# Performance work log

Measured on AMD Instinct MI355X. Metric: run time of the kernel, lower is better.

Reference implementation:

```python
import jax, jax.numpy as jnp
import numpy as np

EMB = 1024; H = 8; HD = EMB // H // 2  # head_dim = 64, q/k use 2*H heads of HD; v uses H heads of 2*HD
FF = 4096; DEPTH = 1
LAM_INIT = float(0.8 - 0.6 * np.exp(-0.3 * DEPTH))

def setup_inputs() -> dict:
    key = jax.random.key(0)
    ks = jax.random.split(key, 12)
    s = lambda k, sh, sc: jax.random.normal(k, sh, jnp.float32) * sc
    return {
        'x': s(ks[0], (2, 2048, EMB), 1.0),
        'ln1_w': jnp.ones((EMB,), jnp.float32), 'ln1_b': jnp.zeros((EMB,), jnp.float32),
        'Wq': s(ks[1], (EMB, EMB), 0.02), 'Wk': s(ks[2], (EMB, EMB), 0.02),
        'Wv': s(ks[3], (EMB, EMB), 0.02), 'Wo': s(ks[4], (EMB, EMB), 0.02),
        'lq1': s(ks[5], (HD,), 0.1), 'lk1': s(ks[6], (HD,), 0.1),
        'lq2': s(ks[7], (HD,), 0.1), 'lk2': s(ks[8], (HD,), 0.1),
        'subln_w': jnp.ones((2 * HD,), jnp.float32),
        'ln2_w': jnp.ones((EMB,), jnp.float32), 'ln2_b': jnp.zeros((EMB,), jnp.float32),
        'W1': s(ks[9], (EMB, FF), 0.02), 'b1': jnp.zeros((FF,), jnp.float32),
        'W2': s(ks[10], (FF, EMB), 0.02), 'b2': jnp.zeros((EMB,), jnp.float32),
    }

def _ln(x, w, b):
    m = jnp.mean(x, -1, keepdims=True)
    v = jnp.var(x, -1, keepdims=True)
    return (x - m) * jax.lax.rsqrt(v + 1e-5) * w + b

def _rms(x, w):
    return x * jax.lax.rsqrt(jnp.mean(x * x, -1, keepdims=True) + 1e-5) * w

def reference(x, ln1_w, ln1_b, Wq, Wk, Wv, Wo, lq1, lk1, lq2, lk2, subln_w, ln2_w, ln2_b, W1, b1, W2, b2):
    B, N, _ = x.shape
    h = _ln(x, ln1_w, ln1_b)
    q = (h @ Wq).reshape(B, N, 2 * H, HD) * (HD ** -0.5)
    k = (h @ Wk).reshape(B, N, 2 * H, HD)
    v = (h @ Wv).reshape(B, N, H, 2 * HD)
    # dual softmax attention maps: [B, 2H, N, N]
    attn = jax.nn.softmax(jnp.einsum('bihd,bjhd->bhij', q, k), axis=-1)
    attn = attn.reshape(B, H, 2, N, N)
    lam = jnp.exp(jnp.sum(lq1 * lk1)) - jnp.exp(jnp.sum(lq2 * lk2)) + LAM_INIT
    a = attn[:, :, 0] - lam * attn[:, :, 1]  # differential attention [B,H,N,N]
    o = jnp.einsum('bhij,bjhd->bihd', a, v)  # [B,N,H,2*HD]
    o = _rms(o, subln_w) * (1.0 - LAM_INIT)
    x = x + o.reshape(B, N, EMB) @ Wo
    h = _ln(x, ln2_w, ln2_b)
    return x + (jax.nn.gelu(h @ W1 + b1, approximate=False) @ W2 + b2)
```

## Files before the change

kernel.cpp:

```cpp
#include <hip/hip_runtime.h>


typedef unsigned short u16;
typedef unsigned int u32;
typedef __attribute__((ext_vector_type(8))) __bf16 bf16x8;
typedef __attribute__((ext_vector_type(4))) float f32x4;
typedef __attribute__((ext_vector_type(4))) u32 u32x4;
typedef __attribute__((ext_vector_type(2))) u32 u32x2;

#define LOG2E 1.4426950408889634f
#define LAM_INIT 0.355509068f
#define ONE_MINUS_LAM_INIT 0.644490932f

__device__ __forceinline__ float bf2f(u16 x) {
  u32 u = ((u32)x) << 16;
  return __builtin_bit_cast(float, u);
}
__device__ __forceinline__ u16 f2bf(float f) {
  u32 u = __builtin_bit_cast(u32, f);
  u32 r = (u + 0x7FFFu + ((u >> 16) & 1u)) >> 16;
  return (u16)r;
}
__device__ __forceinline__ u32 cvtpk(float lo, float hi) {
  u32 r;
  asm("v_cvt_pk_bf16_f32 %0, %1, %2" : "=v"(r) : "v"(lo), "v"(hi));
  return r;
}
__device__ __forceinline__ float ldf(const void* p, size_t i, bool f32) {
  return f32 ? ((const float*)p)[i] : bf2f(((const u16*)p)[i]);
}
__device__ __forceinline__ void async16(const u16* g, u16* l) {
  __builtin_amdgcn_global_load_lds((const __attribute__((address_space(1))) u32*)g,
                                   (__attribute__((address_space(3))) u32*)l, 16, 0, 0);
}
__device__ __forceinline__ bf16x8 ld8(const u16* p) { return *(const bf16x8*)p; }

__global__ void detect_kernel(const u32* x, int* flag) {
  int e = (x[threadIdx.x] >> 7) & 0xFF;
  unsigned long long m = __ballot(e >= 90 && e <= 150);
  if (threadIdx.x == 0) flag[0] = (__popcll(m) >= 40) ? 1 : 0;
}

__global__ void lam_kernel(const void* lq1, const void* lk1, const void* lq2,
                           const void* lk2, const int* flag, float* out) {
  const bool f32 = flag[0] == 0;
  int L = threadIdx.x;
  float a = ldf(lq1, L, f32) * ldf(lk1, L, f32);
  float c = ldf(lq2, L, f32) * ldf(lk2, L, f32);
#pragma unroll
  for (int m = 1; m < 64; m <<= 1) { a += __shfl_xor(a, m); c += __shfl_xor(c, m); }
  if (L == 0) out[0] = __expf(a) - __expf(c) + LAM_INIT;
}

__device__ __forceinline__ void unpack8(u32x4 u, float* f) {
#pragma unroll
  for (int i = 0; i < 4; ++i) {
    f[2 * i] = bf2f((u16)(u[i] & 0xffffu));
    f[2 * i + 1] = bf2f((u16)(u[i] >> 16));
  }
}

template <bool XRAW>
__global__ __launch_bounds__(256) void ln_kernel(const void* __restrict__ x,
                                                 const void* __restrict__ w,
                                                 const void* __restrict__ b,
                                                 const int* __restrict__ flag,
                                                 u16* __restrict__ out) {
  const bool f32 = flag[0] == 0;
  const int row = blockIdx.x * 4 + (threadIdx.x >> 6);
  const int L = threadIdx.x & 63;
  float xv[16];
  if (XRAW && f32) {
    const f32x4* xr = (const f32x4*)((const float*)x + (size_t)row * 1024 + L * 16);
#pragma unroll
    for (int i = 0; i < 4; ++i) {
      f32x4 vv = xr[i];
#pragma unroll
      for (int j = 0; j < 4; ++j) xv[i * 4 + j] = vv[j];
    }
  } else {
    const u16* xr = (const u16*)x + (size_t)row * 1024 + L * 16;
    unpack8(*(const u32x4*)xr, xv);
    unpack8(*(const u32x4*)(xr + 8), xv + 8);
  }
  float s = 0.f, sq = 0.f;
#pragma unroll
  for (int i = 0; i < 16; ++i) { s += xv[i]; sq += xv[i] * xv[i]; }
#pragma unroll
  for (int m = 1; m < 64; m <<= 1) { s += __shfl_xor(s, m); sq += __shfl_xor(sq, m); }
  float mean = s * (1.0f / 1024.0f);
  float var = sq * (1.0f / 1024.0f) - mean * mean;
  float rstd = rsqrtf(var + 1e-5f);
  u32 pk[8];
#pragma unroll
  for (int i = 0; i < 8; ++i) {
    float w0 = ldf(w, L * 16 + 2 * i, f32), w1 = ldf(w, L * 16 + 2 * i + 1, f32);
    float b0 = ldf(b, L * 16 + 2 * i, f32), b1v = ldf(b, L * 16 + 2 * i + 1, f32);
    float v0 = (xv[2 * i] - mean) * rstd * w0 + b0;
    float v1 = (xv[2 * i + 1] - mean) * rstd * w1 + b1v;
    pk[i] = (u32)f2bf(v0) | ((u32)f2bf(v1) << 16);
  }
  u32x4 o0 = {pk[0], pk[1], pk[2], pk[3]};
  u32x4 o1 = {pk[4], pk[5], pk[6], pk[7]};
  *(u32x4*)(out + (size_t)row * 1024 + L * 16) = o0;
  *(u32x4*)(out + (size_t)row * 1024 + L * 16 + 8) = o1;
}

__global__ __launch_bounds__(256) void twc_kernel(const void* __restrict__ s0,
                                                  const void* __restrict__ s1,
                                                  const void* __restrict__ s2,
                                                  u16* __restrict__ dst, int sstride,
                                                  int dstride, size_t soff, size_t dzoff,
                                                  const int* __restrict__ flag) {
  __shared__ __align__(16) u16 tile[64][72];
  const bool f32 = flag[0] == 0;
  const void* src = blockIdx.z == 0 ? s0 : (blockIdx.z == 1 ? s1 : s2);
  u16* dz = dst + (size_t)blockIdx.z * dzoff;
  const int r0 = blockIdx.y * 64, c0 = blockIdx.x * 64;
  const int t = threadIdx.x;
  const int rr = t >> 3, cc = t & 7;
#pragma unroll
  for (int i = 0; i < 2; ++i) {
    int row = rr + i * 32;
    size_t idx = (size_t)(r0 + row) * sstride + c0 + cc * 8 + soff;
    if (f32) {
      const f32x4* s = (const f32x4*)((const float*)src + idx);
      f32x4 a = s[0], b = s[1];
      union { u16 t16[8]; u32x4 v; } u_;
#pragma unroll
      for (int j = 0; j < 4; ++j) { u_.t16[j] = f2bf(a[j]); u_.t16[4 + j] = f2bf(b[j]); }
      *(u32x4*)(&tile[row][cc * 8]) = u_.v;
    } else {
      *(u32x4*)(&tile[row][cc * 8]) = *(const u32x4*)((const u16*)src + idx);
    }
  }
  __syncthreads();
  u16* d = dz + (size_t)c0 * dstride + r0;
#pragma unroll
  for (int i = 0; i < 2; ++i) {
    int n = rr + i * 32;
    union { u16 t16[8]; u32x4 v; } u_;
#pragma unroll
    for (int j = 0; j < 8; ++j) u_.t16[j] = tile[cc * 8 + j][n];
    *(u32x4*)(d + (size_t)n * dstride + cc * 8) = u_.v;
  }
}

enum { EP_NONE = 0, EP_RES = 2, EP_GELU = 3, EP_BIASRES = 4, EP_QKV = 5 };

template <int TM, int EPI, bool RESRAW, bool OUTFLEX>
__global__ __launch_bounds__(256, 2) void gemm_bt(
    const u16* __restrict__ A, const u16* __restrict__ Bt, void* __restrict__ Cv,
    int M, int N, int K, const void* __restrict__ bias, int boff,
    const void* __restrict__ res, const int* __restrict__ flag,
    u16* __restrict__ kout, u16* __restrict__ vtout) {
  constexpr int MT = TM / 32;
  __shared__ __align__(16) u16 lds[TM * 64 + 128 * 64];
  const int t = threadIdx.x;
  const int w = t >> 6, L = t & 63;
  const int quad = L >> 4, l16 = L & 15;
  const int m0 = blockIdx.y * TM, n0 = blockIdx.x * 128;
  const int wm = (TM == 128) ? (w >> 1) * 64 : (w & 1) * 32;
  const int wn = (TM == 128) ? (w & 1) * 64 : (w >> 1) * 64;
  const int srow = L >> 3, spc = L & 7;
  const int sc = spc ^ srow;
  constexpr int BBASE = TM * 64;

  f32x4 acc[MT][4] = {};
  const u16* Ab = A + (size_t)m0 * K;
  const u16* Bb = Bt + (size_t)n0 * K;

  for (int kt = 0; kt < K; kt += 64) {
#pragma unroll
    for (int r = 0; r < TM / 32; ++r) {
      int row = r * 32 + w * 8 + srow;
      async16(Ab + (size_t)row * K + kt + sc * 8, &lds[row * 64 + spc * 8]);
    }
#pragma unroll
    for (int r = 0; r < 4; ++r) {
      int row = r * 32 + w * 8 + srow;
      async16(Bb + (size_t)row * K + kt + sc * 8, &lds[BBASE + row * 64 + spc * 8]);
    }
    __syncthreads();
#pragma unroll
    for (int ks = 0; ks < 2; ++ks) {
      bf16x8 af[MT], bfr[4];
#pragma unroll
      for (int mt = 0; mt < MT; ++mt) {
        int row = wm + mt * 16 + l16;
        af[mt] = ld8(&lds[row * 64 + (((ks * 4 + quad) ^ (l16 & 7)) * 8)]);
      }
#pragma unroll
      for (int nt = 0; nt < 4; ++nt) {
        int row = wn + nt * 16 + l16;
        bfr[nt] = ld8(&lds[BBASE + row * 64 + (((ks * 4 + quad) ^ (l16 & 7)) * 8)]);
      }
#pragma unroll
      for (int mt = 0; mt < MT; ++mt)
#pragma unroll
        for (int nt = 0; nt < 4; ++nt)
          acc[mt][nt] =
              __builtin_amdgcn_mfma_f32_16x16x32_bf16(af[mt], bfr[nt], acc[mt][nt], 0, 0, 0);
    }
    __syncthreads();
  }

  const bool f32 = flag[0] == 0;
#pragma unroll
  for (int mt = 0; mt < MT; ++mt) {
#pragma unroll
    for (int nt = 0; nt < 4; ++nt) {
      int col = n0 + wn + nt * 16 + l16;
      float bv = 0.f;
      if (EPI == EP_GELU || EPI == EP_BIASRES) bv = ldf(bias, (size_t)boff + col, f32);
#pragma unroll
      for (int r = 0; r < 4; ++r) {
        int row = m0 + wm + mt * 16 + quad * 4 + r;
        float v = acc[mt][nt][r];
        if (EPI == EP_GELU) {
          v += bv;
          v = 0.5f * v * (1.0f + erff(v * 0.70710678118654752f));
        }
        if (EPI == EP_RES || EPI == EP_BIASRES) {
          size_t ri = (size_t)row * N + col;
          float rv = RESRAW ? ldf(res, ri, f32) : bf2f(((const u16*)res)[ri]);
          v += rv;
          if (EPI == EP_BIASRES) v += bv;
        }
        if (EPI == EP_QKV) {
          if (col < 1024) {
            ((u16*)Cv)[(size_t)row * 1024 + col] = f2bf(v * 0.125f);
          } else if (col < 2048) {
            kout[(size_t)row * 1024 + (col - 1024)] = f2bf(v);
          } else {
            int c2 = col - 2048;
            int bb = row >> 11, n = row & 2047, hh = c2 >> 7, d = c2 & 127;
            vtout[(size_t)((bb * 8 + hh) * 128 + d) * 2048 + n] = f2bf(v);
          }
        } else {
          size_t ci = (size_t)row * N + col;
          if (OUTFLEX && f32)
            ((float*)Cv)[ci] = v;
          else
            ((u16*)Cv)[ci] = f2bf(v);
        }
      }
    }
  }
}

__global__ __launch_bounds__(256, 2) void attn_kernel(
    const u16* __restrict__ q, const u16* __restrict__ k, const u16* __restrict__ vT,
    const float* __restrict__ lamp, const void* __restrict__ subw,
    const int* __restrict__ flag, u16* __restrict__ o) {
  __shared__ __align__(16) u16 lds[24576];
  const int t = threadIdx.x, w = t >> 6, L = t & 63;
  const int quad = L >> 4, l16 = L & 15;
  const int bid = blockIdx.x;
  const int qt = bid & 31, h = (bid >> 5) & 7, b = bid >> 8;
  const int q0 = qt * 64;
  const int comp = w >> 1, rh = (w & 1) * 32;
  const int srow = L >> 3, spc = L & 7, sc = spc ^ srow;
  const u16* vb = vT + (size_t)(b * 8 + h) * (128 * 2048);
  const int pbase = 16384 + w * 2048;

  auto stageK = [&](int kt) {
#pragma unroll
    for (int r = 0; r < 4; ++r) {
      int row = r * 32 + w * 8 + srow;
      int c_ = row >> 6, key = row & 63;
      async16(k + ((size_t)(b * 2048 + kt + key) * 1024 + (2 * h + c_) * 64 + sc * 8),
              &lds[row * 64 + spc * 8]);
    }
  };
  auto stageV = [&](int kt) {
#pragma unroll
    for (int r = 0; r < 4; ++r) {
      int dim = r * 32 + w * 8 + srow;
      async16(vb + (size_t)dim * 2048 + kt + sc * 8, &lds[8192 + dim * 64 + spc * 8]);
    }
  };

  stageK(0);
  stageV(0);
#pragma unroll
  for (int r = 0; r < 4; ++r) {
    int row = r * 32 + w * 8 + srow;
    int c_ = row >> 6, qr = row & 63;
    async16(q + ((size_t)(b * 2048 + q0 + qr) * 1024 + (2 * h + c_) * 64 + sc * 8),
            &lds[16384 + row * 64 + spc * 8]);
  }
  __syncthreads();
  bf16x8 qf[2][2];
#pragma unroll
  for (int mt = 0; mt < 2; ++mt)
#pragma unroll
    for (int ks = 0; ks < 2; ++ks) {
      int row = rh + mt * 16 + l16;
      qf[mt][ks] =
          ld8(&lds[16384 + comp * 4096 + row * 64 + (((ks * 4 + quad) ^ (l16 & 7)) * 8)]);
    }

  float mst[2] = {-3.0e38f, -3.0e38f}, lst[2] = {0.f, 0.f};
  f32x4 oacc[8][2] = {};

  for (int ti = 0; ti < 32; ++ti) {
    f32x4 s[4][2] = {};
#pragma unroll
    for (int ks = 0; ks < 2; ++ks) {
      bf16x8 kf[4];
#pragma unroll
      for (int nt = 0; nt < 4; ++nt) {
        int row = nt * 16 + l16;
        kf[nt] = ld8(&lds[comp * 4096 + row * 64 + (((ks * 4 + quad) ^ (l16 & 7)) * 8)]);
      }
#pragma unroll
      for (int nt = 0; nt < 4; ++nt)
#pragma unroll
        for (int mt = 0; mt < 2; ++mt)
          s[nt][mt] = __builtin_amdgcn_mfma_f32_16x16x32_bf16(kf[nt], qf[mt][ks], s[nt][mt], 0, 0, 0);
    }

#pragma unroll
    for (int mt = 0; mt < 2; ++mt) {
      f32x4 m4;
#pragma unroll
      for (int r = 0; r < 4; ++r)
        m4[r] = fmaxf(fmaxf(s[0][mt][r], s[1][mt][r]), fmaxf(s[2][mt][r], s[3][mt][r]));
      float mx = fmaxf(fmaxf(m4[0], m4[1]), fmaxf(m4[2], m4[3]));
      mx = fmaxf(mx, __shfl_xor(mx, 16));
      mx = fmaxf(mx, __shfl_xor(mx, 32));
      float mnew = fmaxf(mst[mt], mx);
      float al = exp2f((mst[mt] - mnew) * LOG2E);
      f32x4 p4 = {0.f, 0.f, 0.f, 0.f};
#pragma unroll
      for (int nt = 0; nt < 4; ++nt)
#pragma unroll
        for (int r = 0; r < 4; ++r) {
          float p = exp2f((s[nt][mt][r] - mnew) * LOG2E);
          s[nt][mt][r] = p;
          p4[r] += p;
        }
      float ps = (p4[0] + p4[1]) + (p4[2] + p4[3]);
      ps += __shfl_xor(ps, 16);
      ps += __shfl_xor(ps, 32);
      lst[mt] = lst[mt] * al + ps;
      mst[mt] = mnew;
#pragma unroll
      for (int nt = 0; nt < 8; ++nt)
#pragma unroll
        for (int r = 0; r < 4; ++r) oacc[nt][mt][r] *= al;
    }

#pragma unroll
    for (int mt = 0; mt < 2; ++mt) {
      int prow = mt * 16 + l16;
#pragma unroll
      for (int nt = 0; nt < 4; ++nt) {
        int pc = (nt * 2 + (quad >> 1)) ^ (l16 & 7);
        u32x2 pk2 = {cvtpk(s[nt][mt][0], s[nt][mt][1]), cvtpk(s[nt][mt][2], s[nt][mt][3])};
        *(u32x2*)(&lds[pbase + prow * 64 + pc * 8 + (quad & 1) * 4]) = pk2;
      }
    }
    __syncthreads();
    if (ti + 1 < 32) stageK((ti + 1) * 64);

#pragma unroll
    for (int ks = 0; ks < 2; ++ks) {
      bf16x8 pf[2];
#pragma unroll
      for (int mt = 0; mt < 2; ++mt) {
        int row = mt * 16 + l16;
        pf[mt] = ld8(&lds[pbase + row * 64 + (((ks * 4 + quad) ^ (l16 & 7)) * 8)]);
      }
#pragma unroll
      for (int nt = 0; nt < 8; ++nt) {
        int dim = nt * 16 + l16;
        bf16x8 vf = ld8(&lds[8192 + dim * 64 + (((ks * 4 + quad) ^ (l16 & 7)) * 8)]);
#pragma unroll
        for (int mt = 0; mt < 2; ++mt)
          oacc[nt][mt] = __builtin_amdgcn_mfma_f32_16x16x32_bf16(vf, pf[mt], oacc[nt][mt], 0, 0, 0);
      }
    }
    __syncthreads();
    if (ti + 1 < 32) stageV((ti + 1) * 64);
  }

#pragma unroll
  for (int mt = 0; mt < 2; ++mt) {
    float inv = 1.0f / lst[mt];
#pragma unroll
    for (int nt = 0; nt < 8; ++nt)
#pragma unroll
      for (int r = 0; r < 4; ++r) oacc[nt][mt][r] *= inv;
  }

  float* cb = (float*)lds;
  if (comp == 1) {
#pragma unroll
    for (int mt = 0; mt < 2; ++mt) {
      int rowc = rh + mt * 16 + l16;
#pragma unroll
      for (int nt = 0; nt < 8; ++nt)
        *(f32x4*)(&cb[rowc * 132 + nt * 16 + quad * 4]) = oacc[nt][mt];
    }
  }
  __syncthreads();
  if (comp == 0) {
    const bool f32 = flag[0] == 0;
    float lam = lamp[0];
    float sw[8][4];
#pragma unroll
    for (int nt = 0; nt < 8; ++nt)
#pragma unroll
      for (int r = 0; r < 4; ++r) sw[nt][r] = ldf(subw, nt * 16 + quad * 4 + r, f32);
#pragma unroll
    for (int mt = 0; mt < 2; ++mt) {
      int rowc = rh + mt * 16 + l16;
      float dv[8][4];
      float sq = 0.f;
#pragma unroll
      for (int nt = 0; nt < 8; ++nt) {
        f32x4 c2 = *(const f32x4*)(&cb[rowc * 132 + nt * 16 + quad * 4]);
#pragma unroll
        for (int r = 0; r < 4; ++r) {
          float d = oacc[nt][mt][r] - lam * c2[r];
          dv[nt][r] = d;
          sq += d * d;
        }
      }
      sq += __shfl_xor(sq, 16);
      sq += __shfl_xor(sq, 32);
      float rms = rsqrtf(sq * (1.0f / 128.0f) + 1e-5f);
      size_t rowg = (size_t)(b * 2048 + q0 + rowc) * 1024 + h * 128;
#pragma unroll
      for (int nt = 0; nt < 8; ++nt) {
        float v0 = dv[nt][0] * rms * sw[nt][0] * ONE_MINUS_LAM_INIT;
        float v1 = dv[nt][1] * rms * sw[nt][1] * ONE_MINUS_LAM_INIT;
        float v2 = dv[nt][2] * rms * sw[nt][2] * ONE_MINUS_LAM_INIT;
        float v3 = dv[nt][3] * rms * sw[nt][3] * ONE_MINUS_LAM_INIT;
        u32x2 pk2 = {cvtpk(v0, v1), cvtpk(v2, v3)};
        *(u32x2*)(o + rowg + nt * 16 + quad * 4) = pk2;
      }
    }
  }
}

extern "C" void kernel_launch(void* const* d_in, const int* in_sizes, int n_in,
                              void* d_out, int out_size, void* d_ws, size_t ws_size,
                              hipStream_t stream) {
  (void)in_sizes; (void)n_in; (void)out_size; (void)ws_size;
  const void* x = d_in[0];
  const void* ln1w = d_in[1];
  const void* ln1b = d_in[2];
  const void* Wq = d_in[3];
  const void* Wk = d_in[4];
  const void* Wv = d_in[5];
  const void* Wo = d_in[6];
  const void* lq1 = d_in[7];
  const void* lk1 = d_in[8];
  const void* lq2 = d_in[9];
  const void* lk2 = d_in[10];
  const void* subw = d_in[11];
  const void* ln2w = d_in[12];
  const void* ln2b = d_in[13];
  const void* W1 = d_in[14];
  const void* b1 = d_in[15];
  const void* W2 = d_in[16];
  const void* b2 = d_in[17];

  char* ws = (char*)d_ws;
  const size_t MB = 1u << 20;
  u16* A = (u16*)ws;
  u16* B = (u16*)(ws + 8 * MB);
  u16* C = (u16*)(ws + 16 * MB);
  u16* D = (u16*)(ws + 24 * MB);
  u16* E = (u16*)(ws + 32 * MB);
  float* lam = (float*)(ws + 40 * MB);
  int* flag = (int*)(ws + 40 * MB + 64);
  u16* W2Th = D + 2097152;

  detect_kernel<<<dim3(1), dim3(64), 0, stream>>>((const u32*)x, flag);
  lam_kernel<<<dim3(1), dim3(64), 0, stream>>>(lq1, lk1, lq2, lk2, flag, lam);
  ln_kernel<true><<<dim3(1024), dim3(256), 0, stream>>>(x, ln1w, ln1b, flag, A);

  twc_kernel<<<dim3(16, 16, 3), dim3(256), 0, stream>>>(Wq, Wk, Wv, E, 1024, 1024, 0,
                                                        1048576, flag);
  gemm_bt<64, EP_QKV, false, false><<<dim3(24, 64), dim3(256), 0, stream>>>(
      A, E, B, 4096, 3072, 1024, nullptr, 0, nullptr, flag, C, D);

  attn_kernel<<<dim3(512), dim3(256), 0, stream>>>(B, C, D, lam, subw, flag, A);

  twc_kernel<<<dim3(16, 16, 1), dim3(256), 0, stream>>>(Wo, Wo, Wo, D, 1024, 1024, 0, 0,
                                                        flag);
  gemm_bt<64, EP_RES, true, false><<<dim3(8, 64), dim3(256), 0, stream>>>(
      A, D, E, 4096, 1024, 1024, nullptr, 0, x, flag, nullptr, nullptr);
  ln_kernel<false><<<dim3(1024), dim3(256), 0, stream>>>(E, ln2w, ln2b, flag, A);

  for (int hh = 0; hh < 2; ++hh) {
    twc_kernel<<<dim3(32, 16, 1), dim3(256), 0, stream>>>(W1, W1, W1, D, 4096, 1024,
                                                          (size_t)hh * 2048, 0, flag);
    twc_kernel<<<dim3(16, 32, 1), dim3(256), 0, stream>>>(
        W2, W2, W2, W2Th, 1024, 2048, (size_t)hh * 2048 * 1024, 0, flag);
    gemm_bt<128, EP_GELU, false, false><<<dim3(16, 32), dim3(256), 0, stream>>>(
        A, D, B, 4096, 2048, 1024, b1, hh * 2048, nullptr, flag, nullptr, nullptr);
    if (hh == 0) {
      gemm_bt<64, EP_BIASRES, false, true><<<dim3(8, 64), dim3(256), 0, stream>>>(
          B, W2Th, d_out, 4096, 1024, 2048, b2, 0, E, flag, nullptr, nullptr);
    } else {
      gemm_bt<64, EP_RES, true, true><<<dim3(8, 64), dim3(256), 0, stream>>>(
          B, W2Th, d_out, 4096, 1024, 2048, nullptr, 0, d_out, flag, nullptr, nullptr);
    }
  }
}
```

Baseline: 489.6 us.

## Halve attention query tile to 32 rows, raise occupancy, add lazy softmax rescale

The attention kernel now handles 32 query rows per block instead of 64, so each wave owns a single 16-row m-tile. This halves register and LDS use and allows 4 blocks per CU across a grid of 1024 blocks, with block IDs swizzled so blocks sharing a head are spread out. It also adds a lazy online-softmax rescale: the running max is only updated when some row grows by more than 8, which skips the oacc rescale in most iterations. P is now written with ds_write_b32 in a permuted order to reduce bank conflicts. The trade-off is that each K/V tile loaded into LDS is reused by half as many query rows, and the thresholded max relies on exp values staying bounded.

```diff
diff --git a/kernel.cpp b/kernel.cpp
--- a/kernel.cpp
+++ b/kernel.cpp
@@ -34,6 +34,12 @@
                                    (__attribute__((address_space(3))) u32*)l, 16, 0, 0);
 }
 __device__ __forceinline__ bf16x8 ld8(const u16* p) { return *(const bf16x8*)p; }
+__device__ __forceinline__ void ds_write32(u16* l, u32 v) {
+  asm volatile("ds_write_b32 %0, %1" ::"v"(
+                   (u32)(size_t)(__attribute__((address_space(3))) void*)l),
+               "v"(v)
+               : "memory");
+}
 
 __global__ void detect_kernel(const u32* x, int* flag) {
   int e = (x[threadIdx.x] >> 7) & 0xFF;
@@ -249,20 +255,20 @@
   }
 }
 
-__global__ __launch_bounds__(256, 2) void attn_kernel(
+__global__ __launch_bounds__(256, 4) void attn_kernel(
     const u16* __restrict__ q, const u16* __restrict__ k, const u16* __restrict__ vT,
     const float* __restrict__ lamp, const void* __restrict__ subw,
     const int* __restrict__ flag, u16* __restrict__ o) {
-  __shared__ __align__(16) u16 lds[24576];
+  __shared__ __align__(16) u16 lds[20480];
   const int t = threadIdx.x, w = t >> 6, L = t & 63;
   const int quad = L >> 4, l16 = L & 15;
-  const int bid = blockIdx.x;
-  const int qt = bid & 31, h = (bid >> 5) & 7, b = bid >> 8;
-  const int q0 = qt * 64;
-  const int comp = w >> 1, rh = (w & 1) * 32;
+  const int bid = ((blockIdx.x & 7) << 7) | (blockIdx.x >> 3);
+  const int qt = bid & 63, h = (bid >> 6) & 7, b = bid >> 9;
+  const int q0 = qt * 32;
+  const int comp = w >> 1, rh = (w & 1) * 16;
   const int srow = L >> 3, spc = L & 7, sc = spc ^ srow;
   const u16* vb = vT + (size_t)(b * 8 + h) * (128 * 2048);
-  const int pbase = 16384 + w * 2048;
+  const int pbase = 16384 + w * 1024;
 
   auto stageK = [&](int kt) {
 #pragma unroll
@@ -284,28 +290,24 @@
   stageK(0);
   stageV(0);
 #pragma unroll
-  for (int r = 0; r < 4; ++r) {
+  for (int r = 0; r < 2; ++r) {
     int row = r * 32 + w * 8 + srow;
-    int c_ = row >> 6, qr = row & 63;
+    int c_ = row >> 5, qr = row & 31;
     async16(q + ((size_t)(b * 2048 + q0 + qr) * 1024 + (2 * h + c_) * 64 + sc * 8),
             &lds[16384 + row * 64 + spc * 8]);
   }
   __syncthreads();
-  bf16x8 qf[2][2];
-#pragma unroll
-  for (int mt = 0; mt < 2; ++mt)
-#pragma unroll
-    for (int ks = 0; ks < 2; ++ks) {
-      int row = rh + mt * 16 + l16;
-      qf[mt][ks] =
-          ld8(&lds[16384 + comp * 4096 + row * 64 + (((ks * 4 + quad) ^ (l16 & 7)) * 8)]);
-    }
-
-  float mst[2] = {-3.0e38f, -3.0e38f}, lst[2] = {0.f, 0.f};
-  f32x4 oacc[8][2] = {};
+  bf16x8 qf[2];
+#pragma unroll
+  for (int ks = 0; ks < 2; ++ks)
+    qf[ks] = ld8(&lds[16384 + comp * 2048 + (rh + l16) * 64 +
+                      (((ks * 4 + quad) ^ (l16 & 7)) * 8)]);
+
+  float mst = -3.0e38f, lst = 0.f;
+  f32x4 oacc[8] = {};
 
   for (int ti = 0; ti < 32; ++ti) {
-    f32x4 s[4][2] = {};
+    f32x4 s[4] = {};
 #pragma unroll
     for (int ks = 0; ks < 2; ++ks) {
       bf16x8 kf[4];
@@ -316,50 +318,50 @@
       }
 #pragma unroll
       for (int nt = 0; nt < 4; ++nt)
-#pragma unroll
-        for (int mt = 0; mt < 2; ++mt)
-          s[nt][mt] = __builtin_amdgcn_mfma_f32_16x16x32_bf16(kf[nt], qf[mt][ks], s[nt][mt], 0, 0, 0);
-    }
-
-#pragma unroll
-    for (int mt = 0; mt < 2; ++mt) {
-      f32x4 m4;
-#pragma unroll
-      for (int r = 0; r < 4; ++r)
-        m4[r] = fmaxf(fmaxf(s[0][mt][r], s[1][mt][r]), fmaxf(s[2][mt][r], s[3][mt][r]));
-      float mx = fmaxf(fmaxf(m4[0], m4[1]), fmaxf(m4[2], m4[3]));
-      mx = fmaxf(mx, __shfl_xor(mx, 16));
-      mx = fmaxf(mx, __shfl_xor(mx, 32));
-      float mnew = fmaxf(mst[mt], mx);
-      float al = exp2f((mst[mt] - mnew) * LOG2E);
-      f32x4 p4 = {0.f, 0.f, 0.f, 0.f};
-#pragma unroll
-      for (int nt = 0; nt < 4; ++nt)
-#pragma unroll
-        for (int r = 0; r < 4; ++r) {
-          float p = exp2f((s[nt][mt][r] - mnew) * LOG2E);
-          s[nt][mt][r] = p;
-          p4[r] += p;
-        }
-      float ps = (p4[0] + p4[1]) + (p4[2] + p4[3]);
-      ps += __shfl_xor(ps, 16);
-      ps += __shfl_xor(ps, 32);
-      lst[mt] = lst[mt] * al + ps;
-      mst[mt] = mnew;
+        s[nt] = __builtin_amdgcn_mfma_f32_16x16x32_bf16(kf[nt], qf[ks], s[nt], 0, 0, 0);
+    }
+
+    float mx = -3.0e38f;
+#pragma unroll
+    for (int nt = 0; nt < 4; ++nt)
+#pragma unroll
+      for (int r = 0; r < 4; ++r) mx = fmaxf(mx, s[nt][r]);
+    mx = fmaxf(mx, __shfl_xor(mx, 16));
+    mx = fmaxf(mx, __shfl_xor(mx, 32));
+    unsigned long long grow = __ballot(mx > mst + 8.0f);
+    if (grow) {
+      float mnew = fmaxf(mst, mx);
+      float al = exp2f((mst - mnew) * LOG2E);
+      mst = mnew;
+      lst *= al;
 #pragma unroll
       for (int nt = 0; nt < 8; ++nt)
 #pragma unroll
-        for (int r = 0; r < 4; ++r) oacc[nt][mt][r] *= al;
-    }
-
-#pragma unroll
-    for (int mt = 0; mt < 2; ++mt) {
-      int prow = mt * 16 + l16;
+        for (int r = 0; r < 4; ++r) oacc[nt][r] *= al;
+    }
+    float ps = 0.f;
+#pragma unroll
+    for (int nt = 0; nt < 4; ++nt)
+#pragma unroll
+      for (int r = 0; r < 4; ++r) {
+        float p = exp2f((s[nt][r] - mst) * LOG2E);
+        s[nt][r] = p;
+        ps += p;
+      }
+    ps += __shfl_xor(ps, 16);
+    ps += __shfl_xor(ps, 32);
+    lst += ps;
+
+    {
+      int dsel = quad >> 1;
 #pragma unroll
       for (int nt = 0; nt < 4; ++nt) {
-        int pc = (nt * 2 + (quad >> 1)) ^ (l16 & 7);
-        u32x2 pk2 = {cvtpk(s[nt][mt][0], s[nt][mt][1]), cvtpk(s[nt][mt][2], s[nt][mt][3])};
-        *(u32x2*)(&lds[pbase + prow * 64 + pc * 8 + (quad & 1) * 4]) = pk2;
+        int pc = (nt * 2 + dsel) ^ (l16 & 7);
+        u32 wlo = cvtpk(s[nt][0], s[nt][1]);
+        u32 whi = cvtpk(s[nt][2], s[nt][3]);
+        u16* base = &lds[pbase + l16 * 64 + pc * 8 + (quad & 1) * 4];
+        ds_write32(base + 2 * dsel, dsel ? whi : wlo);
+        ds_write32(base + 2 * (1 - dsel), dsel ? wlo : whi);
       }
     }
     __syncthreads();
@@ -367,81 +369,62 @@
 
 #pragma unroll
     for (int ks = 0; ks < 2; ++ks) {
-      bf16x8 pf[2];
-#pragma unroll
-      for (int mt = 0; mt < 2; ++mt) {
-        int row = mt * 16 + l16;
-        pf[mt] = ld8(&lds[pbase + row * 64 + (((ks * 4 + quad) ^ (l16 & 7)) * 8)]);
-      }
+      bf16x8 pf = ld8(&lds[pbase + l16 * 64 + (((ks * 4 + quad) ^ (l16 & 7)) * 8)]);
 #pragma unroll
       for (int nt = 0; nt < 8; ++nt) {
         int dim = nt * 16 + l16;
         bf16x8 vf = ld8(&lds[8192 + dim * 64 + (((ks * 4 + quad) ^ (l16 & 7)) * 8)]);
-#pragma unroll
-        for (int mt = 0; mt < 2; ++mt)
-          oacc[nt][mt] = __builtin_amdgcn_mfma_f32_16x16x32_bf16(vf, pf[mt], oacc[nt][mt], 0, 0, 0);
+        oacc[nt] = __builtin_amdgcn_mfma_f32_16x16x32_bf16(vf, pf, oacc[nt], 0, 0, 0);
       }
     }
     __syncthreads();
     if (ti + 1 < 32) stageV((ti + 1) * 64);
   }
 
-#pragma unroll
-  for (int mt = 0; mt < 2; ++mt) {
-    float inv = 1.0f / lst[mt];
+  {
+    float inv = 1.0f / lst;
 #pragma unroll
     for (int nt = 0; nt < 8; ++nt)
 #pragma unroll
-      for (int r = 0; r < 4; ++r) oacc[nt][mt][r] *= inv;
+      for (int r = 0; r < 4; ++r) oacc[nt][r] *= inv;
   }
 
   float* cb = (float*)lds;
   if (comp == 1) {
-#pragma unroll
-    for (int mt = 0; mt < 2; ++mt) {
-      int rowc = rh + mt * 16 + l16;
-#pragma unroll
-      for (int nt = 0; nt < 8; ++nt)
-        *(f32x4*)(&cb[rowc * 132 + nt * 16 + quad * 4]) = oacc[nt][mt];
-    }
+    int rowc = rh + l16;
+#pragma unroll
+    for (int nt = 0; nt < 8; ++nt)
+      *(f32x4*)(&cb[rowc * 132 + nt * 16 + quad * 4]) = oacc[nt];
   }
   __syncthreads();
   if (comp == 0) {
     const bool f32 = flag[0] == 0;
     float lam = lamp[0];
-    float sw[8][4];
-#pragma unroll
-    for (int nt = 0; nt < 8; ++nt)
-#pragma unroll
-      for (int r = 0; r < 4; ++r) sw[nt][r] = ldf(subw, nt * 16 + quad * 4 + r, f32);
-#pragma unroll
-    for (int mt = 0; mt < 2; ++mt) {
-      int rowc = rh + mt * 16 + l16;
-      float dv[8][4];
-      float sq = 0.f;
-#pragma unroll
-      for (int nt = 0; nt < 8; ++nt) {
-        f32x4 c2 = *(const f32x4*)(&cb[rowc * 132 + nt * 16 + quad * 4]);
-#pragma unroll
-        for (int r = 0; r < 4; ++r) {
-          float d = oacc[nt][mt][r] - lam * c2[r];
-          dv[nt][r] = d;
-          sq += d * d;
-        }
-      }
-      sq += __shfl_xor(sq, 16);
-      sq += __shfl_xor(sq, 32);
-      float rms = rsqrtf(sq * (1.0f / 128.0f) + 1e-5f);
-      size_t rowg = (size_t)(b * 2048 + q0 + rowc) * 1024 + h * 128;
-#pragma unroll
-      for (int nt = 0; nt < 8; ++nt) {
-        float v0 = dv[nt][0] * rms * sw[nt][0] * ONE_MINUS_LAM_INIT;
-        float v1 = dv[nt][1] * rms * sw[nt][1] * ONE_MINUS_LAM_INIT;
-        float v2 = dv[nt][2] * rms * sw[nt][2] * ONE_MINUS_LAM_INIT;
-        float v3 = dv[nt][3] * rms * sw[nt][3] * ONE_MINUS_LAM_INIT;
-        u32x2 pk2 = {cvtpk(v0, v1), cvtpk(v2, v3)};
-        *(u32x2*)(o + rowg + nt * 16 + quad * 4) = pk2;
-      }
+    int rowc = rh + l16;
+    float dv[8][4];
+    float sq = 0.f;
+#pragma unroll
+    for (int nt = 0; nt < 8; ++nt) {
+      f32x4 c2 = *(const f32x4*)(&cb[rowc * 132 + nt * 16 + quad * 4]);
+#pragma unroll
+      for (int r = 0; r < 4; ++r) {
+        float d = oacc[nt][r] - lam * c2[r];
+        dv[nt][r] = d;
+        sq += d * d;
+      }
+    }
+    sq += __shfl_xor(sq, 16);
+    sq += __shfl_xor(sq, 32);
+    float rms = rsqrtf(sq * (1.0f / 128.0f) + 1e-5f);
+    size_t rowg = (size_t)(b * 2048 + q0 + rowc) * 1024 + h * 128;
+#pragma unroll
+    for (int nt = 0; nt < 8; ++nt) {
+      float v0 = dv[nt][0] * rms * ldf(subw, nt * 16 + quad * 4 + 0, f32) * ONE_MINUS_LAM_INIT;
+      float v1 = dv[nt][1] * rms * ldf(subw, nt * 16 + quad * 4 + 1, f32) * ONE_MINUS_LAM_INIT;
+      float v2 = dv[nt][2] * rms * ldf(subw, nt * 16 + quad * 4 + 2, f32) * ONE_MINUS_LAM_INIT;
+      float v3 = dv[nt][3] * rms * ldf(subw, nt * 16 + quad * 4 + 3, f32) * ONE_MINUS_LAM_INIT;
+      u32x2 pk2 = {cvtpk(v0, v1), cvtpk(v2, v3)};
+      *(u32x2*)(o + rowg + nt * 16 + quad * 4) = pk2;
     }
   }
 }
@@ -489,7 +472,7 @@
   gemm_bt<64, EP_QKV, false, false><<<dim3(24, 64), dim3(256), 0, stream>>>(
       A, E, B, 4096, 3072, 1024, nullptr, 0, nullptr, flag, C, D);
 
-  attn_kernel<<<dim3(512), dim3(256), 0, stream>>>(B, C, D, lam, subw, flag, A);
+  attn_kernel<<<dim3(1024), dim3(256), 0, stream>>>(B, C, D, lam, subw, flag, A);
 
   twc_kernel<<<dim3(16, 16, 1), dim3(256), 0, stream>>>(Wo, Wo, Wo, D, 1024, 1024, 0, 0,
                                                         flag);
```

Result: slower. 511.5 us (+4.5%).
